# Performance work log

Measured on AMD Instinct MI355X. Metric: run time of the kernel, lower is better.

The kernel has to match this reference:

```python
import jax, jax.numpy as jnp
import numpy as np

EMB = 1024
HEADS = 16
HEAD_DIM = EMB // HEADS  # 64


def setup_inputs() -> dict:
    key = jax.random.key(0)
    ks = jax.random.split(key, 11)
    B, S = 2, 2048
    scale = 1.0 / np.sqrt(EMB)
    inp = {
        "xv": jax.random.normal(ks[0], (B, S, EMB), jnp.float32),
        "xk": jax.random.normal(ks[1], (B, S, EMB), jnp.float32),
        "xq": jax.random.normal(ks[2], (B, S, EMB), jnp.float32),
        "Wq": jax.random.normal(ks[3], (EMB, EMB), jnp.float32) * scale,
        "bq": jax.random.normal(ks[4], (EMB,), jnp.float32) * 0.01,
        "Wk": jax.random.normal(ks[5], (EMB, EMB), jnp.float32) * scale,
        "bk": jax.random.normal(ks[6], (EMB,), jnp.float32) * 0.01,
        "Wv": jax.random.normal(ks[7], (EMB, EMB), jnp.float32) * scale,
        "bv": jax.random.normal(ks[8], (EMB,), jnp.float32) * 0.01,
        "Wo": jax.random.normal(ks[9], (EMB, EMB), jnp.float32) * scale,
        "bo": jax.random.normal(ks[10], (EMB,), jnp.float32) * 0.01,
    }
    return inp


def reference(xv, xk, xq, Wq, bq, Wk, bk, Wv, bv, Wo, bo):
    B, S, E = xq.shape
    H, D = HEADS, HEAD_DIM
    # projections (x @ W + b), split into heads: [B,S,H,D]
    Q = (xq @ Wq + bq).reshape(B, S, H, D)
    K = (xk @ Wk + bk).reshape(B, S, H, D)
    V = (xv @ Wv + bv).reshape(B, S, H, D)
    # scaled dot-product attention per head (vectorized over heads)
    scores = jnp.einsum("bqhd,bkhd->bhqk", Q, K) / jnp.sqrt(jnp.float32(D))
    attn = jax.nn.softmax(scores, axis=-1)
    ctx = jnp.einsum("bhqk,bkhd->bqhd", attn, V).reshape(B, S, E)
    return ctx @ Wo + bo
```

## Files before the change

### kernel.cpp

```cpp
#include <hip/hip_runtime.h>
#include <hip/hip_bf16.h>

typedef __hip_bfloat16 bf16;
typedef __attribute__((ext_vector_type(8))) short short8;
typedef __attribute__((ext_vector_type(4))) short short4v;
typedef __attribute__((ext_vector_type(4))) float floatx4;

#define MFMA16 __builtin_amdgcn_mfma_f32_16x16x32_bf16
#define BARRIER __builtin_amdgcn_s_barrier
#define SCHEDB0() __builtin_amdgcn_sched_barrier(0)
#define SETPRIO __builtin_amdgcn_s_setprio


__device__ __forceinline__ void gl16(const void* g, void* l) {
    __builtin_amdgcn_global_load_lds(
        (const __attribute__((address_space(1))) void*)g,
        (__attribute__((address_space(3))) void*)l, 16, 0, 0);
}

__global__ __launch_bounds__(256) void wtrans_k(const float* __restrict__ w0,
                                                const float* __restrict__ w1,
                                                const float* __restrict__ w2,
                                                const float* __restrict__ w3,
                                                bf16* __restrict__ dst) {
    const float* srcs[4] = {w0, w1, w2, w3};
    const float* src = srcs[blockIdx.z];
    bf16* d = dst + (size_t)blockIdx.z * 1024 * 1024;
    __shared__ float t[32][33];
    int tx = threadIdx.x, ty = threadIdx.y;
    int x0 = blockIdx.x * 32, y0 = blockIdx.y * 32;
#pragma unroll
    for (int i = 0; i < 4; i++)
        t[ty + i * 8][tx] = src[(size_t)(y0 + ty + i * 8) * 1024 + x0 + tx];
    __syncthreads();
#pragma unroll
    for (int i = 0; i < 4; i++)
        d[(size_t)(x0 + ty + i * 8) * 1024 + y0 + tx] =
            __float2bfloat16(t[tx][ty + i * 8]);
}

__global__ __launch_bounds__(256) void xcast_k(const float* __restrict__ x0,
                                               const float* __restrict__ x1,
                                               const float* __restrict__ x2,
                                               bf16* __restrict__ dst) {
    const float* srcs[3] = {x0, x1, x2};
    const float* src = srcs[blockIdx.y];
    bf16* d = dst + (size_t)blockIdx.y * (4096 * 1024);
    size_t i = (size_t)blockIdx.x * 256 + threadIdx.x;
    const float4* s4 = (const float4*)src + i * 2;
    float4 a = s4[0], b = s4[1];
    union { __hip_bfloat162 h2[4]; short8 s; } pk;
    pk.h2[0] = __float22bfloat162_rn(make_float2(a.x, a.y));
    pk.h2[1] = __float22bfloat162_rn(make_float2(a.z, a.w));
    pk.h2[2] = __float22bfloat162_rn(make_float2(b.x, b.y));
    pk.h2[3] = __float22bfloat162_rn(make_float2(b.z, b.w));
    *(short8*)&d[i * 8] = pk.s;
}

__global__ __launch_bounds__(256) void qkv_k(const bf16* __restrict__ xb,
                                             const bf16* __restrict__ wt,
                                             const float* __restrict__ bq,
                                             const float* __restrict__ bk,
                                             const float* __restrict__ bv,
                                             bf16* __restrict__ Qw,
                                             bf16* __restrict__ Kw,
                                             bf16* __restrict__ Vt) {
    __shared__ __align__(16) bf16 lA[3][128 * 32];
    __shared__ __align__(16) bf16 lB[3][128 * 32];
    int z = blockIdx.z;
    const bf16* A = xb + (size_t)z * (4096 * 1024);
    const bf16* Bt = wt + (size_t)z * (1024 * 1024);
    const float* bias = (z == 0) ? bq : (z == 1) ? bk : bv;
    int m0 = blockIdx.x * 128, n0 = blockIdx.y * 128;
    int tid = threadIdx.x, wave = tid >> 6, lane = tid & 63;
    int lm = lane & 15, quad = lane >> 4;
    int wm = wave >> 1, wn = wave & 1;
    int swb = quad ^ ((lm >> 1) & 3);

    floatx4 acc[4][4];
#pragma unroll
    for (int i = 0; i < 4; i++)
#pragma unroll
        for (int j = 0; j < 4; j++) acc[i][j] = (floatx4){0.f, 0.f, 0.f, 0.f};

    auto stage = [&](int bufi, int kt) {
#pragma unroll
        for (int q2 = 0; q2 < 2; q2++) {
            int slot0 = wave * 128 + q2 * 64;
            int r = (slot0 + lane) >> 2;
            int c = (lane & 3) ^ ((r >> 1) & 3);
            gl16(&A[(size_t)(m0 + r) * 1024 + kt * 32 + c * 8],
                 &lA[bufi][slot0 * 8]);
            gl16(&Bt[(size_t)(n0 + r) * 1024 + kt * 32 + c * 8],
                 &lB[bufi][slot0 * 8]);
        }
    };

    auto compute = [&](int cur) {
        short8 af[4], bfr[4];
#pragma unroll
        for (int ms = 0; ms < 4; ms++) {
            int r = wm * 64 + ms * 16 + lm;
            af[ms] = *(const short8*)&lA[cur][(r * 4 + swb) * 8];
        }
#pragma unroll
        for (int ns = 0; ns < 4; ns++) {
            int r = wn * 64 + ns * 16 + lm;
            bfr[ns] = *(const short8*)&lB[cur][(r * 4 + swb) * 8];
        }
        SETPRIO(1);
#pragma unroll
        for (int ms = 0; ms < 4; ms++)
#pragma unroll
            for (int ns = 0; ns < 4; ns++)
                acc[ms][ns] = MFMA16(af[ms], bfr[ns], acc[ms][ns], 0, 0, 0);
        SETPRIO(0);
    };

    stage(0, 0);
    stage(1, 1);
    for (int kt = 0; kt < 32; kt++) {
        int cur = kt % 3;
        BARRIER();
        if (kt < 30) {
            stage((kt + 2) % 3, kt + 2);
            asm volatile("s_waitcnt vmcnt(8)" ::: "memory");
        } else if (kt == 30) {
            asm volatile("s_waitcnt vmcnt(4)" ::: "memory");
        } else {
            asm volatile("s_waitcnt vmcnt(0)" ::: "memory");
        }
        BARRIER();
        SCHEDB0();
        compute(cur);
    }

    bf16* dstQK = (z == 0) ? Qw : Kw;
    float scale = (z == 0) ? 0.125f * 1.44269504f : 1.0f;
#pragma unroll
    for (int ms = 0; ms < 4; ms++) {
        int rowb = m0 + wm * 64 + ms * 16 + quad * 4;
        int bb = rowb >> 11, s0 = rowb & 2047;
#pragma unroll
        for (int ns = 0; ns < 4; ns++) {
            int col = n0 + wn * 64 + ns * 16 + lm;
            float bvv = bias[col];
            int hh = col >> 6, d = col & 63;
            if (z < 2) {
#pragma unroll
                for (int rr = 0; rr < 4; rr++) {
                    float v = (acc[ms][ns][rr] + bvv) * scale;
                    dstQK[((((size_t)bb * 16 + hh) * 2048 + s0 + rr) << 6) + d] =
                        __float2bfloat16(v);
                }
            } else {
                short4v pk;
#pragma unroll
                for (int rr = 0; rr < 4; rr++) {
                    bf16 h = __float2bfloat16(acc[ms][ns][rr] + bvv);
                    pk[rr] = *(short*)&h;
                }
                *(short4v*)&Vt[((((size_t)bb * 16 + hh) * 64 + d) << 11) + s0] = pk;
            }
        }
    }
}

__global__ __launch_bounds__(256) void outproj_k(const bf16* __restrict__ ctx,
                                                 const bf16* __restrict__ wot,
                                                 const float* __restrict__ bo,
                                                 float* __restrict__ out) {
    __shared__ __align__(16) bf16 lA[2][128 * 32];
    __shared__ __align__(16) bf16 lB[2][64 * 32];
    int m0 = blockIdx.x * 128, n0 = blockIdx.y * 64;
    int tid = threadIdx.x, wave = tid >> 6, lane = tid & 63;
    int lm = lane & 15, quad = lane >> 4;
    int wm = wave >> 1, wn = wave & 1;
    int swb = quad ^ ((lm >> 1) & 3);

    floatx4 acc[4][2];
#pragma unroll
    for (int i = 0; i < 4; i++)
#pragma unroll
        for (int j = 0; j < 2; j++) acc[i][j] = (floatx4){0.f, 0.f, 0.f, 0.f};

    auto stage = [&](int bufi, int kt) {
#pragma unroll
        for (int q2 = 0; q2 < 2; q2++) {
            int slot0 = wave * 128 + q2 * 64;
            int r = (slot0 + lane) >> 2;
            int c = (lane & 3) ^ ((r >> 1) & 3);
            gl16(&ctx[(size_t)(m0 + r) * 1024 + kt * 32 + c * 8],
                 &lA[bufi][slot0 * 8]);
        }
        {
            int slot0 = wave * 64;
            int r = (slot0 + lane) >> 2;
            int c = (lane & 3) ^ ((r >> 1) & 3);
            gl16(&wot[(size_t)(n0 + r) * 1024 + kt * 32 + c * 8],
                 &lB[bufi][slot0 * 8]);
        }
    };

    auto compute = [&](int cur) {
        short8 af[4], bfr[2];
#pragma unroll
        for (int ms = 0; ms < 4; ms++) {
            int r = wm * 64 + ms * 16 + lm;
            af[ms] = *(const short8*)&lA[cur][(r * 4 + swb) * 8];
        }
#pragma unroll
        for (int ns = 0; ns < 2; ns++) {
            int r = wn * 32 + ns * 16 + lm;
            bfr[ns] = *(const short8*)&lB[cur][(r * 4 + swb) * 8];
        }
        SETPRIO(1);
#pragma unroll
        for (int ms = 0; ms < 4; ms++)
#pragma unroll
            for (int ns = 0; ns < 2; ns++)
                acc[ms][ns] = MFMA16(af[ms], bfr[ns], acc[ms][ns], 0, 0, 0);
        SETPRIO(0);
    };

    stage(0, 0);
    for (int kt = 0; kt < 31; kt++) {
        int cur = kt & 1;
        BARRIER();
        stage(cur ^ 1, kt + 1);
        asm volatile("s_waitcnt vmcnt(3)" ::: "memory");
        BARRIER();
        SCHEDB0();
        compute(cur);
    }
    BARRIER();
    asm volatile("s_waitcnt vmcnt(0)" ::: "memory");
    BARRIER();
    SCHEDB0();
    compute(1);

#pragma unroll
    for (int ms = 0; ms < 4; ms++) {
        int rowb = m0 + wm * 64 + ms * 16 + quad * 4;
#pragma unroll
        for (int ns = 0; ns < 2; ns++) {
            int col = n0 + wn * 32 + ns * 16 + lm;
            float bvv = bo[col];
#pragma unroll
            for (int rr = 0; rr < 4; rr++)
                out[(size_t)(rowb + rr) * 1024 + col] = acc[ms][ns][rr] + bvv;
        }
    }
}

__global__ __launch_bounds__(256) void attn_k(const bf16* __restrict__ Q,
                                              const bf16* __restrict__ K,
                                              const bf16* __restrict__ Vt,
                                              bf16* __restrict__ ctx) {
    __shared__ __align__(16) bf16 lK[2][64 * 64];
    __shared__ __align__(16) bf16 lV[2][64 * 64];
    __shared__ __align__(16) bf16 lP[128 * 64];
    int bh = blockIdx.x, qt = blockIdx.y;
    int b = bh >> 4, h = bh & 15;
    const bf16* Qh = Q + (size_t)bh * (2048 * 64);
    const bf16* Kh = K + (size_t)bh * (2048 * 64);
    const bf16* Vh = Vt + (size_t)bh * (64 * 2048);
    int tid = threadIdx.x, wave = tid >> 6, lane = tid & 63;
    int lm = lane & 15, quad = lane >> 4;
    int s7 = lm & 7;

    short8 qf[2][2];
#pragma unroll
    for (int qh = 0; qh < 2; qh++) {
        int qrow = qt * 128 + wave * 32 + qh * 16 + lm;
        qf[qh][0] = *(const short8*)&Qh[(size_t)qrow * 64 + quad * 8];
        qf[qh][1] = *(const short8*)&Qh[(size_t)qrow * 64 + 32 + quad * 8];
    }

    short8 onesf;
#pragma unroll
    for (int i = 0; i < 8; i++) onesf[i] = (short)0x3F80;

    floatx4 o[2][4];
#pragma unroll
    for (int qh = 0; qh < 2; qh++)
#pragma unroll
        for (int i = 0; i < 4; i++) o[qh][i] = (floatx4){0.f, 0.f, 0.f, 0.f};
    floatx4 accL[2] = {(floatx4){0.f, 0.f, 0.f, 0.f},
                       (floatx4){0.f, 0.f, 0.f, 0.f}};

    auto stage = [&](int bufi, int kt) {
#pragma unroll
        for (int q2 = 0; q2 < 2; q2++) {
            int slot0 = wave * 128 + q2 * 64;
            int r = (slot0 + lane) >> 3;
            int c = (lane & 7) ^ (r & 7);
            gl16(&Kh[(size_t)(kt * 64 + r) * 64 + c * 8], &lK[bufi][slot0 * 8]);
            gl16(&Vh[(size_t)r * 2048 + kt * 64 + c * 8], &lV[bufi][slot0 * 8]);
        }
    };

    char* lPr0 = (char*)lP + (wave * 32 + lm) * 128;
    char* lPr1 = lPr0 + 16 * 128;

    auto compute = [&](int cur) {
        floatx4 s[2][4];
#pragma unroll
        for (int qh = 0; qh < 2; qh++)
#pragma unroll
            for (int i = 0; i < 4; i++) s[qh][i] = (floatx4){0.f, 0.f, 0.f, 0.f};
        SETPRIO(1);
#pragma unroll
        for (int ns = 0; ns < 4; ns++) {
            int r = ns * 16 + lm;
            short8 kf0 = *(const short8*)&lK[cur][(r * 8 + (quad ^ s7)) * 8];
            short8 kf1 = *(const short8*)&lK[cur][(r * 8 + ((4 + quad) ^ s7)) * 8];
            s[0][ns] = MFMA16(kf0, qf[0][0], s[0][ns], 0, 0, 0);
            s[0][ns] = MFMA16(kf1, qf[0][1], s[0][ns], 0, 0, 0);
            s[1][ns] = MFMA16(kf0, qf[1][0], s[1][ns], 0, 0, 0);
            s[1][ns] = MFMA16(kf1, qf[1][1], s[1][ns], 0, 0, 0);
        }
        SETPRIO(0);

#pragma unroll
        for (int qh = 0; qh < 2; qh++) {
            char* pr = qh ? lPr1 : lPr0;
#pragma unroll
            for (int ns = 0; ns < 4; ns++) {
                float p0 = __builtin_amdgcn_exp2f(s[qh][ns][0]);
                float p1 = __builtin_amdgcn_exp2f(s[qh][ns][1]);
                float p2 = __builtin_amdgcn_exp2f(s[qh][ns][2]);
                float p3 = __builtin_amdgcn_exp2f(s[qh][ns][3]);
                union { __hip_bfloat162 h2[2]; short4v s4; } pk;
                pk.h2[0] = __float22bfloat162_rn(make_float2(p0, p1));
                pk.h2[1] = __float22bfloat162_rn(make_float2(p2, p3));
                int sw = (2 * ns + (quad >> 1)) ^ s7;
                *(short4v*)(pr + sw * 16 + (quad & 1) * 8) = pk.s4;
            }
        }

        SETPRIO(1);
#pragma unroll
        for (int kk = 0; kk < 2; kk++) {
            int c2 = (kk * 4 + quad) ^ s7;
            short8 pf0 = *(const short8*)(lPr0 + c2 * 16);
            short8 pf1 = *(const short8*)(lPr1 + c2 * 16);
            accL[0] = MFMA16(pf0, onesf, accL[0], 0, 0, 0);
            accL[1] = MFMA16(pf1, onesf, accL[1], 0, 0, 0);
#pragma unroll
            for (int ns = 0; ns < 4; ns++) {
                int r = ns * 16 + lm;
                short8 vf = *(const short8*)&lV[cur][(r * 8 + ((kk * 4 + quad) ^ s7)) * 8];
                o[0][ns] = MFMA16(pf0, vf, o[0][ns], 0, 0, 0);
                o[1][ns] = MFMA16(pf1, vf, o[1][ns], 0, 0, 0);
            }
        }
        SETPRIO(0);
    };

    stage(0, 0);
    for (int kt = 0; kt < 31; kt++) {
        int cur = kt & 1;
        BARRIER();
        stage(cur ^ 1, kt + 1);
        asm volatile("s_waitcnt vmcnt(4)" ::: "memory");
        BARRIER();
        SCHEDB0();
        compute(cur);
    }
    BARRIER();
    asm volatile("s_waitcnt vmcnt(0)" ::: "memory");
    BARRIER();
    SCHEDB0();
    compute(1);

    float inv[2][4];
#pragma unroll
    for (int qh = 0; qh < 2; qh++)
#pragma unroll
        for (int rr = 0; rr < 4; rr++) inv[qh][rr] = 1.f / accL[qh][rr];

#pragma unroll
    for (int qh = 0; qh < 2; qh++) {
#pragma unroll
        for (int ns = 0; ns < 4; ns++) {
            int e = h * 64 + ns * 16 + lm;
#pragma unroll
            for (int rr = 0; rr < 4; rr++) {
                int srow = qt * 128 + wave * 32 + qh * 16 + quad * 4 + rr;
                ctx[(size_t)(b * 2048 + srow) * 1024 + e] =
                    __float2bfloat16(o[qh][ns][rr] * inv[qh][rr]);
            }
        }
    }
}

extern "C" void kernel_launch(void* const* d_in, const int* in_sizes, int n_in,
                              void* d_out, int out_size, void* d_ws, size_t ws_size,
                              hipStream_t stream) {
    const float* xv = (const float*)d_in[0];
    const float* xk = (const float*)d_in[1];
    const float* xq = (const float*)d_in[2];
    const float* Wq = (const float*)d_in[3];
    const float* bq = (const float*)d_in[4];
    const float* Wk = (const float*)d_in[5];
    const float* bk = (const float*)d_in[6];
    const float* Wv = (const float*)d_in[7];
    const float* bv = (const float*)d_in[8];
    const float* Wo = (const float*)d_in[9];
    const float* bo = (const float*)d_in[10];
    float* out = (float*)d_out;
    bf16* ws = (bf16*)d_ws;

    const size_t MB1 = 1024 * 1024;
    bf16* wt  = ws;
    bf16* Qw  = ws + 4 * MB1;
    bf16* Kw  = ws + 8 * MB1;
    bf16* Vt  = ws + 12 * MB1;
    bf16* ctx = ws + 16 * MB1;
    bf16* xb  = ws + 20 * MB1;

    hipLaunchKernelGGL(wtrans_k, dim3(32, 32, 4), dim3(32, 8), 0, stream,
                       Wq, Wk, Wv, Wo, wt);

    hipLaunchKernelGGL(xcast_k, dim3(2048, 3), dim3(256), 0, stream,
                       xq, xk, xv, xb);

    hipLaunchKernelGGL(qkv_k, dim3(32, 8, 3), dim3(256), 0, stream,
                       xb, wt, bq, bk, bv, Qw, Kw, Vt);

    hipLaunchKernelGGL(attn_k, dim3(32, 16), dim3(256), 0, stream, Qw, Kw, Vt, ctx);

    hipLaunchKernelGGL(outproj_k, dim3(32, 16), dim3(256), 0, stream,
                       ctx, wt + 3 * MB1, bo, out);
}
```

Measured before the change: 219.3 us.

## Split attention waves across key halves and keep P in registers

The attention kernel now assigns each wave 64 query rows and half of each 64-key tile, instead of 32 query rows over the full tile. The score accumulator layout now matches the P operand layout of the PV MFMA, so P stays in registers and the LDS round-trip through the lP buffer is dropped. V fragments are gathered with 8-byte reads to match. The two key-half partial outputs and row sums are reduced through shared memory at the end. This raises register pressure (qf 4x2, o 4x4) and adds a final reduction, while launch bounds now request 2 blocks per CU.

Result: faster. 210.1 us (-4.2%).

```diff
diff --git a/kernel.cpp b/kernel.cpp
--- a/kernel.cpp
+++ b/kernel.cpp
@@ -253,13 +253,12 @@
     }
 }
 
-__global__ __launch_bounds__(256) void attn_k(const bf16* __restrict__ Q,
-                                              const bf16* __restrict__ K,
-                                              const bf16* __restrict__ Vt,
-                                              bf16* __restrict__ ctx) {
-    __shared__ __align__(16) bf16 lK[2][64 * 64];
-    __shared__ __align__(16) bf16 lV[2][64 * 64];
-    __shared__ __align__(16) bf16 lP[128 * 64];
+__global__ __launch_bounds__(256, 2) void attn_k(const bf16* __restrict__ Q,
+                                                 const bf16* __restrict__ K,
+                                                 const bf16* __restrict__ Vt,
+                                                 bf16* __restrict__ ctx) {
+    __shared__ __align__(16) bf16 lKV[2][2][64 * 64];
+    __shared__ float scrL[2][64];
     int bh = blockIdx.x, qt = blockIdx.y;
     int b = bh >> 4, h = bh & 15;
     const bf16* Qh = Q + (size_t)bh * (2048 * 64);
@@ -268,26 +267,28 @@
     int tid = threadIdx.x, wave = tid >> 6, lane = tid & 63;
     int lm = lane & 15, quad = lane >> 4;
     int s7 = lm & 7;
-
-    short8 qf[2][2];
-#pragma unroll
-    for (int qh = 0; qh < 2; qh++) {
-        int qrow = qt * 128 + wave * 32 + qh * 16 + lm;
-        qf[qh][0] = *(const short8*)&Qh[(size_t)qrow * 64 + quad * 8];
-        qf[qh][1] = *(const short8*)&Qh[(size_t)qrow * 64 + 32 + quad * 8];
+    int wq = wave >> 1, wk = wave & 1;
+
+    short8 qf[4][2];
+#pragma unroll
+    for (int qblk = 0; qblk < 4; qblk++) {
+        int qrow = qt * 128 + wq * 64 + qblk * 16 + lm;
+        qf[qblk][0] = *(const short8*)&Qh[(size_t)qrow * 64 + quad * 8];
+        qf[qblk][1] = *(const short8*)&Qh[(size_t)qrow * 64 + 32 + quad * 8];
     }
 
     short8 onesf;
 #pragma unroll
     for (int i = 0; i < 8; i++) onesf[i] = (short)0x3F80;
 
-    floatx4 o[2][4];
-#pragma unroll
-    for (int qh = 0; qh < 2; qh++)
-#pragma unroll
-        for (int i = 0; i < 4; i++) o[qh][i] = (floatx4){0.f, 0.f, 0.f, 0.f};
-    floatx4 accL[2] = {(floatx4){0.f, 0.f, 0.f, 0.f},
-                       (floatx4){0.f, 0.f, 0.f, 0.f}};
+    floatx4 o[4][4];
+#pragma unroll
+    for (int i = 0; i < 4; i++)
+#pragma unroll
+        for (int j = 0; j < 4; j++) o[i][j] = (floatx4){0.f, 0.f, 0.f, 0.f};
+    floatx4 accL[4];
+#pragma unroll
+    for (int i = 0; i < 4; i++) accL[i] = (floatx4){0.f, 0.f, 0.f, 0.f};
 
     auto stage = [&](int bufi, int kt) {
 #pragma unroll
@@ -295,65 +296,75 @@
             int slot0 = wave * 128 + q2 * 64;
             int r = (slot0 + lane) >> 3;
             int c = (lane & 7) ^ (r & 7);
-            gl16(&Kh[(size_t)(kt * 64 + r) * 64 + c * 8], &lK[bufi][slot0 * 8]);
-            gl16(&Vh[(size_t)r * 2048 + kt * 64 + c * 8], &lV[bufi][slot0 * 8]);
-        }
-    };
-
-    char* lPr0 = (char*)lP + (wave * 32 + lm) * 128;
-    char* lPr1 = lPr0 + 16 * 128;
+            gl16(&Kh[(size_t)(kt * 64 + r) * 64 + c * 8], &lKV[0][bufi][slot0 * 8]);
+            gl16(&Vh[(size_t)r * 2048 + kt * 64 + c * 8], &lKV[1][bufi][slot0 * 8]);
+        }
+    };
 
     auto compute = [&](int cur) {
-        floatx4 s[2][4];
-#pragma unroll
-        for (int qh = 0; qh < 2; qh++)
-#pragma unroll
-            for (int i = 0; i < 4; i++) s[qh][i] = (floatx4){0.f, 0.f, 0.f, 0.f};
+        short8 kf[2][2];
+#pragma unroll
+        for (int ksub = 0; ksub < 2; ksub++) {
+            int r = wk * 32 + ksub * 16 + lm;
+#pragma unroll
+            for (int ds = 0; ds < 2; ds++)
+                kf[ksub][ds] = *(const short8*)
+                    &lKV[0][cur][(r * 8 + ((ds * 4 + quad) ^ s7)) * 8];
+        }
+        floatx4 s[4][2];
+#pragma unroll
+        for (int i = 0; i < 4; i++)
+#pragma unroll
+            for (int j = 0; j < 2; j++) s[i][j] = (floatx4){0.f, 0.f, 0.f, 0.f};
         SETPRIO(1);
 #pragma unroll
-        for (int ns = 0; ns < 4; ns++) {
-            int r = ns * 16 + lm;
-            short8 kf0 = *(const short8*)&lK[cur][(r * 8 + (quad ^ s7)) * 8];
-            short8 kf1 = *(const short8*)&lK[cur][(r * 8 + ((4 + quad) ^ s7)) * 8];
-            s[0][ns] = MFMA16(kf0, qf[0][0], s[0][ns], 0, 0, 0);
-            s[0][ns] = MFMA16(kf1, qf[0][1], s[0][ns], 0, 0, 0);
-            s[1][ns] = MFMA16(kf0, qf[1][0], s[1][ns], 0, 0, 0);
-            s[1][ns] = MFMA16(kf1, qf[1][1], s[1][ns], 0, 0, 0);
-        }
+        for (int qblk = 0; qblk < 4; qblk++)
+#pragma unroll
+            for (int ksub = 0; ksub < 2; ksub++) {
+                s[qblk][ksub] = MFMA16(kf[ksub][0], qf[qblk][0], s[qblk][ksub], 0, 0, 0);
+                s[qblk][ksub] = MFMA16(kf[ksub][1], qf[qblk][1], s[qblk][ksub], 0, 0, 0);
+            }
         SETPRIO(0);
 
-#pragma unroll
-        for (int qh = 0; qh < 2; qh++) {
-            char* pr = qh ? lPr1 : lPr0;
-#pragma unroll
-            for (int ns = 0; ns < 4; ns++) {
-                float p0 = __builtin_amdgcn_exp2f(s[qh][ns][0]);
-                float p1 = __builtin_amdgcn_exp2f(s[qh][ns][1]);
-                float p2 = __builtin_amdgcn_exp2f(s[qh][ns][2]);
-                float p3 = __builtin_amdgcn_exp2f(s[qh][ns][3]);
-                union { __hip_bfloat162 h2[2]; short4v s4; } pk;
-                pk.h2[0] = __float22bfloat162_rn(make_float2(p0, p1));
-                pk.h2[1] = __float22bfloat162_rn(make_float2(p2, p3));
-                int sw = (2 * ns + (quad >> 1)) ^ s7;
-                *(short4v*)(pr + sw * 16 + (quad & 1) * 8) = pk.s4;
+        short8 pz[4];
+#pragma unroll
+        for (int qblk = 0; qblk < 4; qblk++) {
+            union { short4v h[2]; short8 s8; } up;
+#pragma unroll
+            for (int ksub = 0; ksub < 2; ksub++) {
+                float p0 = __builtin_amdgcn_exp2f(s[qblk][ksub][0]);
+                float p1 = __builtin_amdgcn_exp2f(s[qblk][ksub][1]);
+                float p2 = __builtin_amdgcn_exp2f(s[qblk][ksub][2]);
+                float p3 = __builtin_amdgcn_exp2f(s[qblk][ksub][3]);
+                union { __hip_bfloat162 b2[2]; short4v s4; } c;
+                c.b2[0] = __float22bfloat162_rn(make_float2(p0, p1));
+                c.b2[1] = __float22bfloat162_rn(make_float2(p2, p3));
+                up.h[ksub] = c.s4;
             }
+            pz[qblk] = up.s8;
+        }
+
+        short8 vfz[4];
+#pragma unroll
+        for (int dblk = 0; dblk < 4; dblk++) {
+            int d = dblk * 16 + lm;
+            union { short4v h[2]; short8 s8; } uv;
+#pragma unroll
+            for (int ksub = 0; ksub < 2; ksub++) {
+                int g = 4 * wk + 2 * ksub + (quad >> 1);
+                uv.h[ksub] = *(const short4v*)
+                    &lKV[1][cur][(d * 8 + (g ^ s7)) * 8 + (quad & 1) * 4];
+            }
+            vfz[dblk] = uv.s8;
         }
 
         SETPRIO(1);
 #pragma unroll
-        for (int kk = 0; kk < 2; kk++) {
-            int c2 = (kk * 4 + quad) ^ s7;
-            short8 pf0 = *(const short8*)(lPr0 + c2 * 16);
-            short8 pf1 = *(const short8*)(lPr1 + c2 * 16);
-            accL[0] = MFMA16(pf0, onesf, accL[0], 0, 0, 0);
-            accL[1] = MFMA16(pf1, onesf, accL[1], 0, 0, 0);
-#pragma unroll
-            for (int ns = 0; ns < 4; ns++) {
-                int r = ns * 16 + lm;
-                short8 vf = *(const short8*)&lV[cur][(r * 8 + ((kk * 4 + quad) ^ s7)) * 8];
-                o[0][ns] = MFMA16(pf0, vf, o[0][ns], 0, 0, 0);
-                o[1][ns] = MFMA16(pf1, vf, o[1][ns], 0, 0, 0);
-            }
+        for (int qblk = 0; qblk < 4; qblk++) {
+            accL[qblk] = MFMA16(pz[qblk], onesf, accL[qblk], 0, 0, 0);
+#pragma unroll
+            for (int dblk = 0; dblk < 4; dblk++)
+                o[qblk][dblk] = MFMA16(pz[qblk], vfz[dblk], o[qblk][dblk], 0, 0, 0);
         }
         SETPRIO(0);
     };
@@ -374,22 +385,43 @@
     SCHEDB0();
     compute(1);
 
-    float inv[2][4];
-#pragma unroll
-    for (int qh = 0; qh < 2; qh++)
-#pragma unroll
-        for (int rr = 0; rr < 4; rr++) inv[qh][rr] = 1.f / accL[qh][rr];
-
-#pragma unroll
-    for (int qh = 0; qh < 2; qh++) {
-#pragma unroll
-        for (int ns = 0; ns < 4; ns++) {
-            int e = h * 64 + ns * 16 + lm;
-#pragma unroll
-            for (int rr = 0; rr < 4; rr++) {
-                int srow = qt * 128 + wave * 32 + qh * 16 + quad * 4 + rr;
-                ctx[(size_t)(b * 2048 + srow) * 1024 + e] =
-                    __float2bfloat16(o[qh][ns][rr] * inv[qh][rr]);
+    __syncthreads();
+    float* scrO = (float*)&lKV[0][0][0];
+    if (wk == 1) {
+#pragma unroll
+        for (int qblk = 0; qblk < 4; qblk++) {
+#pragma unroll
+            for (int dblk = 0; dblk < 4; dblk++)
+#pragma unroll
+                for (int rr = 0; rr < 4; rr++)
+                    scrO[wq * 4096 + (qblk * 16 + quad * 4 + rr) * 64 +
+                         dblk * 16 + lm] = o[qblk][dblk][rr];
+#pragma unroll
+            for (int rr = 0; rr < 4; rr++)
+                scrL[wq][qblk * 16 + quad * 4 + rr] = accL[qblk][rr];
+        }
+    }
+    __syncthreads();
+    if (wk == 0) {
+#pragma unroll
+        for (int qblk = 0; qblk < 4; qblk++) {
+            float inv[4];
+#pragma unroll
+            for (int rr = 0; rr < 4; rr++)
+                inv[rr] = 1.f / (accL[qblk][rr] +
+                                 scrL[wq][qblk * 16 + quad * 4 + rr]);
+#pragma unroll
+            for (int dblk = 0; dblk < 4; dblk++) {
+                int e = h * 64 + dblk * 16 + lm;
+#pragma unroll
+                for (int rr = 0; rr < 4; rr++) {
+                    int srow = qt * 128 + wq * 64 + qblk * 16 + quad * 4 + rr;
+                    float of = o[qblk][dblk][rr] +
+                               scrO[wq * 4096 + (qblk * 16 + quad * 4 + rr) * 64 +
+                                    dblk * 16 + lm];
+                    ctx[(size_t)(b * 2048 + srow) * 1024 + e] =
+                        __float2bfloat16(of * inv[rr]);
+                }
             }
         }
     }
```
